# Kernel tuning notes

Hardware: AMD Instinct MI355X
Metric: run time of the kernel (lower is better)

## Reference

```python
import jax, jax.numpy as jnp
import numpy as np

DEPTH = 12
EMB = 768
HEADS = 12
HEAD_DIM = EMB // HEADS
FF = 4 * EMB
EPS = 1e-6
SCALE = HEAD_DIM ** -0.5


def _layernorm(x, w, b):
    mu = jnp.mean(x, axis=-1, keepdims=True)
    var = jnp.mean(jnp.square(x - mu), axis=-1, keepdims=True)
    return (x - mu) * jax.lax.rsqrt(var + EPS) * w + b


def setup_inputs() -> dict:
    key = jax.random.key(0)
    ks = jax.random.split(key, 13)
    s = 0.02
    d = {
        "x": jax.random.normal(ks[0], (8, 1024, EMB), dtype=jnp.float32),
        "ln1_w": jnp.ones((DEPTH, EMB), jnp.float32),
        "ln1_b": jnp.zeros((DEPTH, EMB), jnp.float32),
        "qkv_w": jax.random.normal(ks[1], (DEPTH, EMB, 3 * EMB), jnp.float32) * s,
        "qkv_b": jnp.zeros((DEPTH, 3 * EMB), jnp.float32),
        "proj_w": jax.random.normal(ks[2], (DEPTH, EMB, EMB), jnp.float32) * s,
        "proj_b": jnp.zeros((DEPTH, EMB), jnp.float32),
        "ln2_w": jnp.ones((DEPTH, EMB), jnp.float32),
        "ln2_b": jnp.zeros((DEPTH, EMB), jnp.float32),
        "fc1_w": jax.random.normal(ks[3], (DEPTH, EMB, FF), jnp.float32) * s,
        "fc1_b": jnp.zeros((DEPTH, FF), jnp.float32),
        "fc2_w": jax.random.normal(ks[4], (DEPTH, FF, EMB), jnp.float32) * s,
        "fc2_b": jnp.zeros((DEPTH, EMB), jnp.float32),
    }
    return d


def _block(x, p):
    (l1w, l1b, qw, qb, pw, pb, l2w, l2b, f1w, f1b, f2w, f2b) = p
    B, N, C = x.shape
    # --- attention sub-block (pre-LN, residual add) ---
    h = _layernorm(x, l1w, l1b)
    qkv = (h @ qw + qb).reshape(B, N, 3, HEADS, HEAD_DIM)
    qkv = jnp.transpose(qkv, (2, 0, 3, 1, 4))  # [3,B,H,N,D]
    q, k, v = qkv[0], qkv[1], qkv[2]
    att = jnp.einsum('bhqd,bhkd->bhqk', q, k) * SCALE
    att = jax.nn.softmax(att, axis=-1)
    out = jnp.einsum('bhqk,bhkd->bhqd', att, v)
    out = jnp.transpose(out, (0, 2, 1, 3)).reshape(B, N, C)
    x = x + (out @ pw + pb)
    # --- feed-forward sub-block ---
    h = _layernorm(x, l2w, l2b)
    h = jax.nn.gelu(h @ f1w + f1b, approximate=False)  # nn.GELU default = exact
    x = x + (h @ f2w + f2b)
    return x, None


def reference(x, ln1_w, ln1_b, qkv_w, qkv_b, proj_w, proj_b,
              ln2_w, ln2_b, fc1_w, fc1_b, fc2_w, fc2_b):
    params = (ln1_w, ln1_b, qkv_w, qkv_b, proj_w, proj_b,
              ln2_w, ln2_b, fc1_w, fc1_b, fc2_w, fc2_b)
    out, _ = jax.lax.scan(_block, x, params)
    return out
```

## Files before the change

### kernel.cpp

```cpp
#include <hip/hip_runtime.h>
#include <cstdint>
#include <cstddef>

#define NLAYER 12
#define EMB 768
#define NH 12
#define HD 64
#define FF 3072
#define SEQ 1024
#define BATCH 8
#define NTOK (BATCH * SEQ)

typedef unsigned short ushort_t;
typedef __attribute__((ext_vector_type(8))) short short8;
typedef __attribute__((ext_vector_type(4))) float floatx4;

typedef __attribute__((address_space(1))) void GV;
typedef __attribute__((address_space(3))) void LV;

__device__ __forceinline__ void async16(const void* g, void* l) {
  __builtin_amdgcn_global_load_lds((GV*)g, (LV*)l, 16, 0, 0);
}

__device__ __forceinline__ ushort_t f2bf(float f) {
  union { float f; unsigned u; } a; a.f = f;
  unsigned u = a.u;
  return (ushort_t)((u + 0x7fffu + ((u >> 16) & 1u)) >> 16);
}

__global__ __launch_bounds__(256) void kw_transpose(const float* __restrict__ src,
                                                    ushort_t* __restrict__ dst,
                                                    int K, int N) {
  size_t ls = (size_t)K * N;
  src += (size_t)blockIdx.z * ls;
  dst += (size_t)blockIdx.z * ls;
  int n0 = blockIdx.x * 64, k0 = blockIdx.y * 64;
  __shared__ ushort_t t[64][72];
  int tid = threadIdx.x;
  int r = tid >> 2, c0 = (tid & 3) * 16;
  const float* s = src + (size_t)(k0 + r) * N + n0 + c0;
#pragma unroll
  for (int j = 0; j < 16; j += 4) {
    float4 v = *(const float4*)(s + j);
    t[r][c0 + j + 0] = f2bf(v.x);
    t[r][c0 + j + 1] = f2bf(v.y);
    t[r][c0 + j + 2] = f2bf(v.z);
    t[r][c0 + j + 3] = f2bf(v.w);
  }
  __syncthreads();
  int n = tid >> 2;
  int kk0 = (tid & 3) * 16;
  ushort_t* d = dst + (size_t)(n0 + n) * K + k0 + kk0;
#pragma unroll
  for (int j = 0; j < 16; j += 8) {
    alignas(16) ushort_t tmp[8];
#pragma unroll
    for (int jj = 0; jj < 8; ++jj) tmp[jj] = t[kk0 + j + jj][n];
    *(uint4*)(d + j) = *(const uint4*)tmp;
  }
}

__global__ __launch_bounds__(256) void ln_kernel(const float* __restrict__ x,
                                                 const float* __restrict__ w,
                                                 const float* __restrict__ b,
                                                 ushort_t* __restrict__ out) {
  int wv = threadIdx.x >> 6, lane = threadIdx.x & 63;
  int row = blockIdx.x * 4 + wv;
  const float* xr = x + (size_t)row * EMB;
  float4 v[3];
  float s = 0.f, s2 = 0.f;
#pragma unroll
  for (int k = 0; k < 3; ++k) {
    v[k] = *(const float4*)(xr + lane * 4 + k * 256);
    s += v[k].x + v[k].y + v[k].z + v[k].w;
    s2 += v[k].x * v[k].x + v[k].y * v[k].y + v[k].z * v[k].z + v[k].w * v[k].w;
  }
#pragma unroll
  for (int off = 32; off > 0; off >>= 1) {
    s += __shfl_xor(s, off, 64);
    s2 += __shfl_xor(s2, off, 64);
  }
  float mu = s * (1.f / EMB);
  float var = s2 * (1.f / EMB) - mu * mu;
  float inv = rsqrtf(var + 1e-6f);
  ushort_t* orow = out + (size_t)row * EMB;
#pragma unroll
  for (int k = 0; k < 3; ++k) {
    int c = lane * 4 + k * 256;
    float4 wv4 = *(const float4*)(w + c);
    float4 bv4 = *(const float4*)(b + c);
    alignas(8) ushort_t t4[4];
    t4[0] = f2bf((v[k].x - mu) * inv * wv4.x + bv4.x);
    t4[1] = f2bf((v[k].y - mu) * inv * wv4.y + bv4.y);
    t4[2] = f2bf((v[k].z - mu) * inv * wv4.z + bv4.z);
    t4[3] = f2bf((v[k].w - mu) * inv * wv4.w + bv4.w);
    *(uint2*)(orow + c) = *(const uint2*)t4;
  }
}

__global__ __launch_bounds__(256) void v_transpose(const ushort_t* __restrict__ V,
                                                   ushort_t* __restrict__ Vt) {
  int bh = blockIdx.y, n0 = blockIdx.x * 64;
  const ushort_t* src = V + ((size_t)bh * SEQ + n0) * HD;
  ushort_t* dst = Vt + (size_t)bh * HD * SEQ;
  __shared__ ushort_t t[64][72];
  int tid = threadIdx.x;
#pragma unroll
  for (int i = 0; i < 2; ++i) {
    int c = tid + i * 256;
    int n = c >> 3, doff = (c & 7) * 8;
    *(uint4*)&t[n][doff] = *(const uint4*)(src + (size_t)n * HD + doff);
  }
  __syncthreads();
#pragma unroll
  for (int i = 0; i < 2; ++i) {
    int c = tid + i * 256;
    int d = c >> 3, noff = (c & 7) * 8;
    alignas(16) ushort_t tmp[8];
#pragma unroll
    for (int j = 0; j < 8; ++j) tmp[j] = t[noff + j][d];
    *(uint4*)(dst + (size_t)d * SEQ + n0 + noff) = *(const uint4*)tmp;
  }
}

template <int MODE, int TN>
__global__ __launch_bounds__(256) void gemm_kernel(
    const ushort_t* __restrict__ A, const ushort_t* __restrict__ Bt,
    int K, int N, const float* __restrict__ bias,
    const float* __restrict__ resid, float* __restrict__ outf,
    ushort_t* __restrict__ outb,
    ushort_t* __restrict__ qo, ushort_t* __restrict__ ko, ushort_t* __restrict__ vo) {
  constexpr int MT = (TN == 128) ? 4 : 2;
  __shared__ ushort_t sA[128 * 32];
  __shared__ ushort_t sB[TN * 32];
  __shared__ float sE[4 * 16 * 68];

  int tid = threadIdx.x;
  int wv = tid >> 6, lane = tid & 63;
  int lm = lane & 15, lq = lane >> 4;
  int wm = (TN == 128) ? (wv >> 1) : wv;
  int wn = (TN == 128) ? (wv & 1) : 0;
  int m0 = blockIdx.y * 128, n0 = blockIdx.x * TN;

  floatx4 acc[MT][4] = {};

  const ushort_t* Abase = A + (size_t)m0 * K;
  const ushort_t* Bbase = Bt + (size_t)n0 * K;

  int kIters = K >> 5;
  for (int kt = 0; kt < kIters; ++kt) {
    int kOff = kt * 32;
#pragma unroll
    for (int i = 0; i < 2; ++i) {
      int c = wv * 64 + i * 256 + lane;
      int row = c >> 2, off = (c & 3) * 8;
      async16(Abase + (size_t)row * K + kOff + off, sA + (wv * 64 + i * 256) * 8);
    }
    if (TN == 128) {
#pragma unroll
      for (int i = 0; i < 2; ++i) {
        int c = wv * 64 + i * 256 + lane;
        int row = c >> 2, off = (c & 3) * 8;
        async16(Bbase + (size_t)row * K + kOff + off, sB + (wv * 64 + i * 256) * 8);
      }
    } else {
      int c = wv * 64 + lane;
      int row = c >> 2, off = (c & 3) * 8;
      async16(Bbase + (size_t)row * K + kOff + off, sB + (wv * 64) * 8);
    }
    __syncthreads();
    short8 aF[MT], bF[4];
#pragma unroll
    for (int mt = 0; mt < MT; ++mt)
      aF[mt] = *(const short8*)(sA + (wm * (16 * MT) + mt * 16 + lm) * 32 + lq * 8);
#pragma unroll
    for (int nt = 0; nt < 4; ++nt)
      bF[nt] = *(const short8*)(sB + (wn * 64 + nt * 16 + lm) * 32 + lq * 8);
#pragma unroll
    for (int mt = 0; mt < MT; ++mt)
#pragma unroll
      for (int nt = 0; nt < 4; ++nt)
        acc[mt][nt] = __builtin_amdgcn_mfma_f32_16x16x32_bf16(aF[mt], bF[nt], acc[mt][nt], 0, 0, 0);
    __syncthreads();
  }

  float* eW = sE + wv * (16 * 68);
#pragma unroll
  for (int mt = 0; mt < MT; ++mt) {
#pragma unroll
    for (int nt = 0; nt < 4; ++nt)
#pragma unroll
      for (int r = 0; r < 4; ++r)
        eW[(lq * 4 + r) * 68 + nt * 16 + lm] = acc[mt][nt][r];
    __syncthreads();
    int gm_base = m0 + wm * (16 * MT) + mt * 16;
#pragma unroll
    for (int p = 0; p < 4; ++p) {
      int r16 = p * 4 + lq;
      int gm = gm_base + r16;
      int cc = lm * 4;
      int gn = n0 + wn * 64 + cc;
      float4 vv = *(float4*)(eW + r16 * 68 + cc);
      float4 bb = *(const float4*)(bias + gn);
      if (MODE == 1) {
        float4 rr = *(const float4*)(resid + (size_t)gm * N + gn);
        vv.x += bb.x + rr.x; vv.y += bb.y + rr.y;
        vv.z += bb.z + rr.z; vv.w += bb.w + rr.w;
        *(float4*)(outf + (size_t)gm * N + gn) = vv;
      } else if (MODE == 2) {
        float g0 = vv.x + bb.x, g1 = vv.y + bb.y, g2 = vv.z + bb.z, g3 = vv.w + bb.w;
        alignas(8) ushort_t t4[4];
        t4[0] = f2bf(0.5f * g0 * (1.f + erff(g0 * 0.70710678118654752f)));
        t4[1] = f2bf(0.5f * g1 * (1.f + erff(g1 * 0.70710678118654752f)));
        t4[2] = f2bf(0.5f * g2 * (1.f + erff(g2 * 0.70710678118654752f)));
        t4[3] = f2bf(0.5f * g3 * (1.f + erff(g3 * 0.70710678118654752f)));
        *(uint2*)(outb + (size_t)gm * N + gn) = *(const uint2*)t4;
      } else {
        int which = gn / 768;
        int rem = gn - which * 768;
        int h = rem >> 6, dd = rem & 63;
        float sc = (which == 0) ? 0.125f * 1.44269504088896341f : 1.0f;
        ushort_t* base = (which == 0) ? qo : (which == 1) ? ko : vo;
        int bidx = gm >> 10, nn = gm & 1023;
        alignas(8) ushort_t t4[4];
        t4[0] = f2bf((vv.x + bb.x) * sc);
        t4[1] = f2bf((vv.y + bb.y) * sc);
        t4[2] = f2bf((vv.z + bb.z) * sc);
        t4[3] = f2bf((vv.w + bb.w) * sc);
        *(uint2*)(base + ((size_t)((bidx * NH + h) * SEQ + nn)) * HD + dd) = *(const uint2*)t4;
      }
    }
    __syncthreads();
  }
}

__global__ __launch_bounds__(256, 3) void attn_kernel(const ushort_t* __restrict__ Q,
                                                      const ushort_t* __restrict__ Kin,
                                                      const ushort_t* __restrict__ Vt,
                                                      ushort_t* __restrict__ O) {
  __shared__ ushort_t sK[2 * 64 * 32];
  __shared__ ushort_t sV[2][2 * 64 * 32];
  __shared__ ushort_t sP[4 * 32 * 72];

  int flat = blockIdx.x;
  int xcd = flat & 7, idx = flat >> 3;
  int bh = ((idx >> 3) << 3) + xcd;
  int qb = idx & 7;

  int tid = threadIdx.x, wv = tid >> 6, lane = tid & 63;
  int lm = lane & 15, lq = lane >> 4;

  const ushort_t* Qp = Q + ((size_t)bh * SEQ + qb * 128 + wv * 32) * HD;
  const ushort_t* Kp = Kin + (size_t)bh * SEQ * HD;
  const ushort_t* Vp = Vt + (size_t)bh * HD * SEQ;

  short8 qF[2][2];
#pragma unroll
  for (int mi = 0; mi < 2; ++mi)
#pragma unroll
    for (int kd = 0; kd < 2; ++kd)
      qF[mi][kd] = *(const short8*)(Qp + (size_t)(mi * 16 + lm) * HD + kd * 32 + lq * 8);

#pragma unroll
  for (int i = 0; i < 2; ++i) {
    int s = i * 256 + wv * 64 + lane;
    int kd = s >> 8, row = (s >> 2) & 63, q = s & 3;
    async16(Kp + (size_t)row * HD + kd * 32 + q * 8, sK + (i * 256 + wv * 64) * 8);
  }
#pragma unroll
  for (int i = 0; i < 2; ++i) {
    int s = i * 256 + wv * 64 + lane;
    int ks = s >> 8, d = (s >> 2) & 63, q = s & 3;
    async16(Vp + (size_t)d * SEQ + ks * 32 + q * 8, sV[0] + (i * 256 + wv * 64) * 8);
  }
  __syncthreads();

  floatx4 oF[2][4] = {};
  float mrow[2][4], lrow[2][4];
#pragma unroll
  for (int mi = 0; mi < 2; ++mi)
#pragma unroll
    for (int r = 0; r < 4; ++r) { mrow[mi][r] = -1e30f; lrow[mi][r] = 0.f; }
  ushort_t* Pw = sP + wv * (32 * 72);

  for (int kt = 0; kt < SEQ / 64; ++kt) {
    const ushort_t* sVc = sV[kt & 1];
    floatx4 sF[2][4];
#pragma unroll
    for (int mi = 0; mi < 2; ++mi)
#pragma unroll
      for (int nt = 0; nt < 4; ++nt) sF[mi][nt] = floatx4{0.f, 0.f, 0.f, 0.f};
#pragma unroll
    for (int nt = 0; nt < 4; ++nt) {
      short8 kF0 = *(const short8*)(sK + (0 * 64 + nt * 16 + lm) * 32 + lq * 8);
      short8 kF1 = *(const short8*)(sK + (1 * 64 + nt * 16 + lm) * 32 + lq * 8);
#pragma unroll
      for (int mi = 0; mi < 2; ++mi) {
        sF[mi][nt] = __builtin_amdgcn_mfma_f32_16x16x32_bf16(qF[mi][0], kF0, sF[mi][nt], 0, 0, 0);
        sF[mi][nt] = __builtin_amdgcn_mfma_f32_16x16x32_bf16(qF[mi][1], kF1, sF[mi][nt], 0, 0, 0);
      }
    }
    __syncthreads();

    int nk = (kt < SEQ / 64 - 1) ? kt + 1 : kt;
    ushort_t* sVn = sV[(kt + 1) & 1];
#pragma unroll
    for (int i = 0; i < 2; ++i) {
      int s = i * 256 + wv * 64 + lane;
      int kd = s >> 8, row = (s >> 2) & 63, q = s & 3;
      async16(Kp + (size_t)(nk * 64 + row) * HD + kd * 32 + q * 8, sK + (i * 256 + wv * 64) * 8);
    }
#pragma unroll
    for (int i = 0; i < 2; ++i) {
      int s = i * 256 + wv * 64 + lane;
      int ks = s >> 8, d = (s >> 2) & 63, q = s & 3;
      async16(Vp + (size_t)d * SEQ + nk * 64 + ks * 32 + q * 8, sVn + (i * 256 + wv * 64) * 8);
    }

#pragma unroll
    for (int mi = 0; mi < 2; ++mi) {
#pragma unroll
      for (int r = 0; r < 4; ++r) {
        float mx = fmaxf(fmaxf(sF[mi][0][r], sF[mi][1][r]), fmaxf(sF[mi][2][r], sF[mi][3][r]));
#pragma unroll
        for (int off = 1; off < 16; off <<= 1) mx = fmaxf(mx, __shfl_xor(mx, off, 64));
        float mnew = fmaxf(mrow[mi][r], mx);
        float alpha = __builtin_amdgcn_exp2f(mrow[mi][r] - mnew);
        mrow[mi][r] = mnew;
        float rs = 0.f;
        int prow = (mi * 16 + lq * 4 + r) * 72;
#pragma unroll
        for (int nt = 0; nt < 4; ++nt) {
          float p = __builtin_amdgcn_exp2f(sF[mi][nt][r] - mnew);
          rs += p;
          Pw[prow + nt * 16 + lm] = f2bf(p);
        }
        lrow[mi][r] = lrow[mi][r] * alpha + rs;
#pragma unroll
        for (int dt = 0; dt < 4; ++dt) oF[mi][dt][r] *= alpha;
      }
    }

#pragma unroll
    for (int ks = 0; ks < 2; ++ks) {
      short8 pF[2];
#pragma unroll
      for (int mi = 0; mi < 2; ++mi)
        pF[mi] = *(const short8*)(Pw + (mi * 16 + lm) * 72 + ks * 32 + lq * 8);
#pragma unroll
      for (int dt = 0; dt < 4; ++dt) {
        short8 vF = *(const short8*)(sVc + (ks * 64 + dt * 16 + lm) * 32 + lq * 8);
#pragma unroll
        for (int mi = 0; mi < 2; ++mi)
          oF[mi][dt] = __builtin_amdgcn_mfma_f32_16x16x32_bf16(pF[mi], vF, oF[mi][dt], 0, 0, 0);
      }
    }
    __syncthreads();
  }

#pragma unroll
  for (int mi = 0; mi < 2; ++mi)
#pragma unroll
    for (int r = 0; r < 4; ++r)
#pragma unroll
      for (int off = 1; off < 16; off <<= 1)
        lrow[mi][r] += __shfl_xor(lrow[mi][r], off, 64);

  int b = bh / NH, h = bh - b * NH;
#pragma unroll
  for (int mi = 0; mi < 2; ++mi) {
#pragma unroll
    for (int r = 0; r < 4; ++r) {
      float invl = 1.0f / lrow[mi][r];
      int t = b * SEQ + qb * 128 + wv * 32 + mi * 16 + lq * 4 + r;
      ushort_t* orow = O + (size_t)t * EMB + h * HD;
#pragma unroll
      for (int dt = 0; dt < 4; ++dt) orow[dt * 16 + lm] = f2bf(oF[mi][dt][r] * invl);
    }
  }
}

extern "C" void kernel_launch(void* const* d_in, const int* in_sizes, int n_in,
                              void* d_out, int out_size, void* d_ws, size_t ws_size,
                              hipStream_t stream) {
  const float* xin = (const float*)d_in[0];
  const float* ln1_w = (const float*)d_in[1];
  const float* ln1_b = (const float*)d_in[2];
  const float* qkv_w = (const float*)d_in[3];
  const float* qkv_b = (const float*)d_in[4];
  const float* proj_w = (const float*)d_in[5];
  const float* proj_b = (const float*)d_in[6];
  const float* ln2_w = (const float*)d_in[7];
  const float* ln2_b = (const float*)d_in[8];
  const float* fc1_w = (const float*)d_in[9];
  const float* fc1_b = (const float*)d_in[10];
  const float* fc2_w = (const float*)d_in[11];
  const float* fc2_b = (const float*)d_in[12];

  size_t off = 0;
  char* ws = (char*)d_ws;
  auto alloc = [&](size_t bytes) -> void* {
    void* p = ws + off;
    off += (bytes + 255) & ~(size_t)255;
    return p;
  };
  ushort_t* wt_qkv = (ushort_t*)alloc((size_t)NLAYER * 2304 * 768 * 2);
  ushort_t* wt_proj = (ushort_t*)alloc((size_t)NLAYER * 768 * 768 * 2);
  ushort_t* wt_fc1 = (ushort_t*)alloc((size_t)NLAYER * 3072 * 768 * 2);
  ushort_t* wt_fc2 = (ushort_t*)alloc((size_t)NLAYER * 768 * 3072 * 2);
  float* X = (float*)alloc((size_t)NTOK * EMB * 4);
  ushort_t* Hb = (ushort_t*)alloc((size_t)NTOK * EMB * 2);
  ushort_t* Qb = (ushort_t*)alloc((size_t)NTOK * EMB * 2 * 4);
  ushort_t* Kb = Qb + (size_t)NTOK * EMB;
  ushort_t* Vb = Kb + (size_t)NTOK * EMB;
  ushort_t* Vtb = Vb + (size_t)NTOK * EMB;
  ushort_t* G = Qb;
  ushort_t* AO = (ushort_t*)alloc((size_t)NTOK * EMB * 2);

  hipMemcpyAsync(X, xin, (size_t)NTOK * EMB * 4, hipMemcpyDeviceToDevice, stream);

  dim3 b256(256);
  kw_transpose<<<dim3(36, 12, NLAYER), b256, 0, stream>>>(qkv_w, wt_qkv, 768, 2304);
  kw_transpose<<<dim3(12, 12, NLAYER), b256, 0, stream>>>(proj_w, wt_proj, 768, 768);
  kw_transpose<<<dim3(48, 12, NLAYER), b256, 0, stream>>>(fc1_w, wt_fc1, 768, 3072);
  kw_transpose<<<dim3(12, 48, NLAYER), b256, 0, stream>>>(fc2_w, wt_fc2, 3072, 768);

  for (int l = 0; l < NLAYER; ++l) {
    ln_kernel<<<NTOK / 4, b256, 0, stream>>>(X, ln1_w + l * 768, ln1_b + l * 768, Hb);
    gemm_kernel<0, 128><<<dim3(18, 64), b256, 0, stream>>>(
        Hb, wt_qkv + (size_t)l * 2304 * 768, 768, 2304, qkv_b + l * 2304,
        nullptr, nullptr, nullptr, Qb, Kb, Vb);
    v_transpose<<<dim3(16, 96), b256, 0, stream>>>(Vb, Vtb);
    attn_kernel<<<768, b256, 0, stream>>>(Qb, Kb, Vtb, AO);
    gemm_kernel<1, 64><<<dim3(12, 64), b256, 0, stream>>>(
        AO, wt_proj + (size_t)l * 768 * 768, 768, 768, proj_b + l * 768,
        X, X, nullptr, nullptr, nullptr, nullptr);
    ln_kernel<<<NTOK / 4, b256, 0, stream>>>(X, ln2_w + l * 768, ln2_b + l * 768, Hb);
    gemm_kernel<2, 128><<<dim3(24, 64), b256, 0, stream>>>(
        Hb, wt_fc1 + (size_t)l * 768 * 3072, 768, 3072, fc1_b + l * 3072,
        nullptr, nullptr, G, nullptr, nullptr, nullptr);
    float* outPtr = (l == NLAYER - 1) ? (float*)d_out : X;
    gemm_kernel<1, 64><<<dim3(12, 64), b256, 0, stream>>>(
        G, wt_fc2 + (size_t)l * 3072 * 768, 3072, 768, fc2_b + l * 768,
        X, outPtr, nullptr, nullptr, nullptr, nullptr);
  }
}
```

Baseline: 4.131 ms.

## Double-buffer GEMM LDS tiles and remap blocks across XCDs

```diff
diff --git a/kernel.cpp b/kernel.cpp
--- a/kernel.cpp
+++ b/kernel.cpp
@@ -131,44 +131,64 @@
     ushort_t* __restrict__ outb,
     ushort_t* __restrict__ qo, ushort_t* __restrict__ ko, ushort_t* __restrict__ vo) {
   constexpr int MT = (TN == 128) ? 4 : 2;
-  __shared__ ushort_t sA[128 * 32];
-  __shared__ ushort_t sB[TN * 32];
-  __shared__ float sE[4 * 16 * 68];
+  constexpr int AELE = 128 * 32;
+  constexpr int BELE = TN * 32;
+  constexpr int BUFELE = AELE + BELE;
+  __shared__ alignas(16) ushort_t smem[2 * BUFELE];
 
   int tid = threadIdx.x;
   int wv = tid >> 6, lane = tid & 63;
   int lm = lane & 15, lq = lane >> 4;
   int wm = (TN == 128) ? (wv >> 1) : wv;
   int wn = (TN == 128) ? (wv & 1) : 0;
-  int m0 = blockIdx.y * 128, n0 = blockIdx.x * TN;
-
-  floatx4 acc[MT][4] = {};
+
+  int Gx = gridDim.x;
+  int hw = blockIdx.y * Gx + blockIdx.x;
+  int xcd = hw & 7;
+  int j = hw >> 3;
+  int jq = j / Gx;
+  int by = xcd + (jq << 3);
+  int bx = j - jq * Gx;
+  int m0 = by * 128, n0 = bx * TN;
 
   const ushort_t* Abase = A + (size_t)m0 * K;
   const ushort_t* Bbase = Bt + (size_t)n0 * K;
 
-  int kIters = K >> 5;
-  for (int kt = 0; kt < kIters; ++kt) {
+  auto stage = [&](int buf, int kt) {
+    ushort_t* dA = smem + buf * BUFELE;
+    ushort_t* dB = dA + AELE;
     int kOff = kt * 32;
 #pragma unroll
     for (int i = 0; i < 2; ++i) {
       int c = wv * 64 + i * 256 + lane;
       int row = c >> 2, off = (c & 3) * 8;
-      async16(Abase + (size_t)row * K + kOff + off, sA + (wv * 64 + i * 256) * 8);
+      async16(Abase + (size_t)row * K + kOff + off, dA + (wv * 64 + i * 256) * 8);
     }
     if (TN == 128) {
 #pragma unroll
       for (int i = 0; i < 2; ++i) {
         int c = wv * 64 + i * 256 + lane;
         int row = c >> 2, off = (c & 3) * 8;
-        async16(Bbase + (size_t)row * K + kOff + off, sB + (wv * 64 + i * 256) * 8);
+        async16(Bbase + (size_t)row * K + kOff + off, dB + (wv * 64 + i * 256) * 8);
       }
     } else {
       int c = wv * 64 + lane;
       int row = c >> 2, off = (c & 3) * 8;
-      async16(Bbase + (size_t)row * K + kOff + off, sB + (wv * 64) * 8);
-    }
-    __syncthreads();
+      async16(Bbase + (size_t)row * K + kOff + off, dB + (wv * 64) * 8);
+    }
+  };
+
+  floatx4 acc[MT][4] = {};
+  int kIters = K >> 5;
+
+  stage(0, 0);
+  __syncthreads();
+
+  for (int kt = 0; kt < kIters; ++kt) {
+    int cur = kt & 1;
+    if (kt + 1 < kIters) stage(cur ^ 1, kt + 1);
+    const ushort_t* sA = smem + cur * BUFELE;
+    const ushort_t* sB = sA + AELE;
     short8 aF[MT], bF[4];
 #pragma unroll
     for (int mt = 0; mt < MT; ++mt)
@@ -184,6 +204,7 @@
     __syncthreads();
   }
 
+  float* sE = (float*)smem;
   float* eW = sE + wv * (16 * 68);
 #pragma unroll
   for (int mt = 0; mt < MT; ++mt) {
```

After: 3.834 ms. -7.2%, faster.
